# Performance work log

Measured on AMD Instinct MI355X. Metric: run time of the kernel, lower is better.

## Reference

```python
import jax, jax.numpy as jnp
import numpy as np

DIM = 256
HEADS = 8
HD = DIM // HEADS
SR = 2
SCALE = HD ** -0.5
EPS = 1e-5


def _layernorm(t, g, b):
    m = jnp.mean(t, axis=-1, keepdims=True)
    v = jnp.mean((t - m) ** 2, axis=-1, keepdims=True)
    return (t - m) / jnp.sqrt(v + EPS) * g + b


def _sr_kv(t, H, W, sr_w, sr_b, ln_g, ln_b, Wkv):
    # t: [B, N, C] with N == H*W -> spatial-reduction conv -> LN -> kv proj
    B, N, C = t.shape
    img = t.transpose(0, 2, 1).reshape(B, C, H, W)
    red = jax.lax.conv_general_dilated(
        img, sr_w, window_strides=(SR, SR), padding='VALID',
        dimension_numbers=('NCHW', 'OIHW', 'NCHW')) + sr_b[None, :, None, None]
    red = red.reshape(B, C, -1).transpose(0, 2, 1)  # [B, Nr, C]
    red = _layernorm(red, ln_g, ln_b)
    Nr = red.shape[1]
    kv = (red @ Wkv).reshape(B, Nr, 2, HEADS, HD).transpose(2, 0, 3, 1, 4)
    return kv[0], kv[1]  # k, v: [B, h, Nr, d]


def _q_heads(t, Wq):
    B, N, _ = t.shape
    return (t @ Wq).reshape(B, N, HEADS, HD).transpose(0, 2, 1, 3)  # [B,h,N,d]


def _attn_out(q, k, v, proj_w, proj_b):
    a = jnp.einsum('bhqd,bhkd->bhqk', q, k) * SCALE
    a = jax.nn.softmax(a, axis=-1)
    o = jnp.einsum('bhqk,bhkd->bhqd', a, v)
    B, h, N, d = o.shape
    return o.transpose(0, 2, 1, 3).reshape(B, N, h * d) @ proj_w + proj_b


def _forward(x, y, Wq, Wkv, sr_w, sr_b, ln_g, ln_b, proj_w, proj_b,
             H_x, W_x, H_y, W_y):
    # B_x == 1 branch of the original module (static shapes)
    B_y = y.shape[0]
    q_x = _q_heads(x, Wq)
    q_y = _q_heads(y, Wq)
    k_x, v_x = _sr_kv(x, H_x, W_x, sr_w, sr_b, ln_g, ln_b, Wkv)
    k_y, v_y = _sr_kv(y, H_y, W_y, sr_w, sr_b, ln_g, ln_b, Wkv)
    # x attends to its own KV + batch-averaged support KV
    k_cat_x = jnp.concatenate([k_x, jnp.mean(k_y, axis=0, keepdims=True)], axis=2)
    v_cat_x = jnp.concatenate([v_x, jnp.mean(v_y, axis=0, keepdims=True)], axis=2)
    x_out = _attn_out(q_x, k_cat_x, v_cat_x, proj_w, proj_b)
    # each support attends to repeated query KV + its own KV
    k_cat_y = jnp.concatenate([jnp.broadcast_to(k_x, (B_y,) + k_x.shape[1:]), k_y], axis=2)
    v_cat_y = jnp.concatenate([jnp.broadcast_to(v_x, (B_y,) + v_x.shape[1:]), v_y], axis=2)
    y_out = _attn_out(q_y, k_cat_y, v_cat_y, proj_w, proj_b)
    return x_out, y_out


def setup_inputs() -> dict:
    key = jax.random.key(0)
    ks = jax.random.split(key, 6)
    std = 0.02
    return {
        'x': jax.random.normal(ks[0], (1, 6400, DIM), jnp.float32),
        'y': jax.random.normal(ks[1], (4, 1024, DIM), jnp.float32),
        'Wq': jax.random.normal(ks[2], (DIM, DIM), jnp.float32) * std,
        'Wkv': jax.random.normal(ks[3], (DIM, 2 * DIM), jnp.float32) * std,
        'sr_w': jax.random.normal(ks[4], (DIM, DIM, SR, SR), jnp.float32) * np.sqrt(2.0 / (SR * SR * DIM)),
        'sr_b': jnp.zeros((DIM,), jnp.float32),
        'ln_g': jnp.ones((DIM,), jnp.float32),
        'ln_b': jnp.zeros((DIM,), jnp.float32),
        'proj_w': jax.random.normal(ks[5], (DIM, DIM), jnp.float32) * std,
        'proj_b': jnp.zeros((DIM,), jnp.float32),
        'H_x': 80, 'W_x': 80, 'H_y': 32, 'W_y': 32,
    }


def reference(x, y, Wq, Wkv, sr_w, sr_b, ln_g, ln_b, proj_w, proj_b,
              H_x, W_x, H_y, W_y):
    return _forward(x, y, Wq, Wkv, sr_w, sr_b, ln_g, ln_b, proj_w, proj_b,
                    H_x, W_x, H_y, W_y)
```

## Files before the change

kernel.cpp:

```cpp
#include <hip/hip_runtime.h>
#include <math.h>

#define DIM 256
#define HD 32
#define KSCALE (0.17677669529663687f * 1.44269504088896340736f)
#define EPS 1e-5f

typedef __attribute__((ext_vector_type(8))) short short8;
typedef __attribute__((ext_vector_type(4))) float f32x4;

union U8 { uint4 u; short8 s; };

__device__ inline unsigned short f2bf(float f) {
    union { float f; unsigned u; } v; v.f = f;
    unsigned r = v.u + 0x7FFF + ((v.u >> 16) & 1);
    return (unsigned short)(r >> 16);
}
__device__ inline float bf2f(unsigned short h) {
    union { unsigned u; float f; } v; v.u = ((unsigned)h) << 16;
    return v.f;
}
__device__ inline unsigned pk2bf(float a, float b) {
    unsigned ua = __float_as_uint(a) + 0x8000u;
    unsigned ub = __float_as_uint(b) + 0x8000u;
    return __builtin_amdgcn_perm(ub, ua, 0x07060302u);
}
__device__ inline uint4 pk8bf(float4 a, float4 b) {
    return make_uint4(pk2bf(a.x, a.y), pk2bf(a.z, a.w),
                      pk2bf(b.x, b.y), pk2bf(b.z, b.w));
}
__device__ inline void up2(unsigned u, float& a, float& b) {
    a = __uint_as_float(u << 16);
    b = __uint_as_float(u & 0xffff0000u);
}
__device__ inline void gl_lds16(const unsigned short* g, unsigned short* l) {
    __builtin_amdgcn_global_load_lds(
        (const __attribute__((address_space(1))) unsigned int*)g,
        (__attribute__((address_space(3))) unsigned int*)l, 16, 0, 0);
}
#define MFMA16(a, b, c) __builtin_amdgcn_mfma_f32_16x16x32_bf16(a, b, c, 0, 0, 0)
#define EXP2(x) __builtin_amdgcn_exp2f(x)

__global__ __launch_bounds__(256) void prep_w(
    const float* __restrict__ Wq, const float* __restrict__ Wkv,
    const float* __restrict__ projw, const float* __restrict__ srw,
    unsigned short* __restrict__ WqT, unsigned short* __restrict__ WkvT,
    unsigned short* __restrict__ projT, unsigned short* __restrict__ BwT,
    unsigned short* __restrict__ pads)
{
    int idx = blockIdx.x * 256 + threadIdx.x;
    if (idx < 65536) { int n = idx >> 8, k = idx & 255; WqT[idx] = f2bf(Wq[(k << 8) + n]); return; }
    idx -= 65536;
    if (idx < 131072) { int n = idx >> 8, k = idx & 255; WkvT[idx] = f2bf(Wkv[(k << 9) + n]); return; }
    idx -= 131072;
    if (idx < 65536) { int n = idx >> 8, k = idx & 255; projT[idx] = f2bf(projw[(k << 8) + n]); return; }
    idx -= 65536;
    if (idx < 262144) { int o = idx >> 10, rem = idx & 1023, q = rem >> 8, i = rem & 255;
                        BwT[idx] = f2bf(srw[(o << 10) + (i << 2) + q]); return; }
    idx -= 262144;
    pads[idx] = 0;
}

__global__ __launch_bounds__(256) void convq_kernel(
    const float* __restrict__ x, const float* __restrict__ y,
    const unsigned short* __restrict__ BwT, const unsigned short* __restrict__ WqT,
    unsigned short* __restrict__ redA, unsigned short* __restrict__ redB,
    unsigned short* __restrict__ qxb, unsigned short* __restrict__ qyb)
{
    __shared__ __align__(16) unsigned short At[128][32];
    __shared__ __align__(16) unsigned short Btile[64][32];
    const int tid = threadIdx.x;
    const int lane = tid & 63, w = tid >> 6;
    const int c = lane & 15, quad = lane >> 4;
    const int bid = blockIdx.x;

    if (bid < 328) {
        const int n0 = (bid & 3) << 6, r = bid >> 2;
        const float* Xb; int W, W2, m0g, pl, kh;
        if (r < 50) {
            const int myi = r >> 1; kh = r & 1;
            Xb = x; W = 80; W2 = 40; m0g = myi * 64; pl = myi * 64;
        } else {
            const int ry = r - 50, idx = ry >> 1; kh = ry & 1;
            const int b = idx >> 2, mt = idx & 3;
            Xb = y + (size_t)b * 262144; W = 32; W2 = 16;
            m0g = 1600 + b * 256 + mt * 64; pl = mt * 64;
        }
        unsigned short* Cb = (kh == 0) ? redA : redB;
        const int srow = tid >> 2, sch = (tid & 3) << 3;
        const int p = pl + srow;
        const int oy = p / W2, ox = p - oy * W2;
        const unsigned short* Bp = BwT + (size_t)(n0 + srow) * 1024 + sch;
        const int kbeg = kh << 9, kend = kbeg + 512;

        auto addrA = [&](int k0) {
            const int qq = k0 >> 8;
            const int rrow = (2 * oy + (qq >> 1)) * W + 2 * ox + (qq & 1);
            return Xb + (size_t)rrow * DIM + (k0 & 255) + sch;
        };

        const float* ap = addrA(kbeg);
        float4 a0 = *(const float4*)ap, a1 = *(const float4*)(ap + 4);
        uint4 bn = *(const uint4*)(Bp + kbeg);
        f32x4 acc[4] = {};
        for (int k0 = kbeg; k0 < kend; k0 += 32) {
            *(uint4*)&At[srow][sch]    = pk8bf(a0, a1);
            *(uint4*)&Btile[srow][sch] = bn;
            if (k0 < kend - 32) {
                const float* np = addrA(k0 + 32);
                a0 = *(const float4*)np; a1 = *(const float4*)(np + 4);
                bn = *(const uint4*)(Bp + k0 + 32);
            }
            __syncthreads();
            short8 a = *(short8*)&At[(w << 4) + c][quad << 3];
            #pragma unroll
            for (int nb = 0; nb < 4; ++nb) {
                short8 b = *(short8*)&Btile[(nb << 4) + c][quad << 3];
                acc[nb] = MFMA16(a, b, acc[nb]);
            }
            __syncthreads();
        }
        const int rl = (w << 4) + (quad << 2);
        #pragma unroll
        for (int nb = 0; nb < 4; ++nb) {
            const int col = n0 + (nb << 4) + c;
            #pragma unroll
            for (int rr = 0; rr < 4; ++rr)
                Cb[(size_t)(m0g + rl + rr) * DIM + col] = f2bf(acc[nb][rr]);
        }
    } else {
        const int r = bid - 328;
        const int n0 = (r & 3) << 6, mg = (r >> 2) << 7;
        const float* Ab = (mg < 6400) ? x + (size_t)mg * 256
                                      : y + (size_t)(mg - 6400) * 256;
        unsigned short* Cb = (mg < 6400) ? qxb + (size_t)mg * 256
                                         : qyb + (size_t)(mg - 6400) * 256;
        const int arow = tid >> 1, ach = (tid & 1) << 4;
        const float* Ap = Ab + (size_t)arow * 256 + ach;
        const int brow = tid >> 2, bch = (tid & 3) << 3;
        const unsigned short* Bp = WqT + (size_t)(n0 + brow) * 256 + bch;

        float4 a0 = *(const float4*)Ap,       a1 = *(const float4*)(Ap + 4);
        float4 a2 = *(const float4*)(Ap + 8), a3 = *(const float4*)(Ap + 12);
        uint4 bn = *(const uint4*)Bp;
        f32x4 acc[2][4] = {};
        for (int k0 = 0; k0 < 256; k0 += 32) {
            *(uint4*)&At[arow][ach]     = pk8bf(a0, a1);
            *(uint4*)&At[arow][ach + 8] = pk8bf(a2, a3);
            *(uint4*)&Btile[brow][bch]  = bn;
            if (k0 < 224) {
                a0 = *(const float4*)(Ap + k0 + 32); a1 = *(const float4*)(Ap + k0 + 36);
                a2 = *(const float4*)(Ap + k0 + 40); a3 = *(const float4*)(Ap + k0 + 44);
                bn = *(const uint4*)(Bp + k0 + 32);
            }
            __syncthreads();
            #pragma unroll
            for (int ml = 0; ml < 2; ++ml) {
                short8 a = *(short8*)&At[(w << 5) + (ml << 4) + c][quad << 3];
                #pragma unroll
                for (int nb = 0; nb < 4; ++nb) {
                    short8 b = *(short8*)&Btile[(nb << 4) + c][quad << 3];
                    acc[ml][nb] = MFMA16(a, b, acc[ml][nb]);
                }
            }
            __syncthreads();
        }
        #pragma unroll
        for (int ml = 0; ml < 2; ++ml) {
            const int rl = (w << 5) + (ml << 4) + (quad << 2);
            #pragma unroll
            for (int nb = 0; nb < 4; ++nb) {
                const int col = n0 + (nb << 4) + c;
                #pragma unroll
                for (int rr = 0; rr < 4; ++rr)
                    Cb[(size_t)(rl + rr) * 256 + col] = f2bf(acc[ml][nb][rr]);
            }
        }
    }
}

__global__ __launch_bounds__(256) void kvln_kernel(
    const unsigned short* __restrict__ redA, const unsigned short* __restrict__ redB,
    const unsigned short* __restrict__ WkvT, const float* __restrict__ srb,
    const float* __restrict__ g, const float* __restrict__ bta,
    unsigned short* __restrict__ kswx, unsigned short* __restrict__ vswx,
    unsigned short* __restrict__ kswy, unsigned short* __restrict__ vswy)
{
    __shared__ __align__(16) unsigned short At[64][32];
    __shared__ __align__(16) unsigned short Btile[64][32];
    const int tid = threadIdx.x;
    const int lane = tid & 63, w = tid >> 6;
    const int c = lane & 15, quad = lane >> 4;
    const int srow = tid >> 2, sch = (tid & 3) << 3;
    const int bid = blockIdx.x;
    const int n0 = (bid & 7) << 6, mg = (bid >> 3) << 6;
    const unsigned short* ArowA = redA + (size_t)(mg + srow) * 256 + sch;
    const unsigned short* ArowB = redB + (size_t)(mg + srow) * 256 + sch;

    uint4 araw[8];
    float s1 = 0.f, s2 = 0.f;
    #pragma unroll
    for (int ci = 0; ci < 8; ++ci) {
        uint4 ua = *(const uint4*)(ArowA + (ci << 5));
        uint4 ub = *(const uint4*)(ArowB + (ci << 5));
        const int ch = (ci << 5) + sch;
        float4 sb0 = *(const float4*)(srb + ch), sb1 = *(const float4*)(srb + ch + 4);
        const unsigned* dua = (const unsigned*)&ua;
        const unsigned* dub = (const unsigned*)&ub;
        float t[8];
        #pragma unroll
        for (int dd = 0; dd < 4; ++dd) {
            float a0, a1, b0, b1;
            up2(dua[dd], a0, a1); up2(dub[dd], b0, b1);
            t[2 * dd]     = a0 + b0;
            t[2 * dd + 1] = a1 + b1;
        }
        t[0] += sb0.x; t[1] += sb0.y; t[2] += sb0.z; t[3] += sb0.w;
        t[4] += sb1.x; t[5] += sb1.y; t[6] += sb1.z; t[7] += sb1.w;
        #pragma unroll
        for (int j = 0; j < 8; ++j) { s1 += t[j]; s2 += t[j] * t[j]; }
        araw[ci] = pk8bf(make_float4(t[0], t[1], t[2], t[3]),
                         make_float4(t[4], t[5], t[6], t[7]));
    }
    s1 += __shfl_xor(s1, 1); s1 += __shfl_xor(s1, 2);
    s2 += __shfl_xor(s2, 1); s2 += __shfl_xor(s2, 2);
    const float mean = s1 * (1.0f / 256.0f);
    const float var  = s2 * (1.0f / 256.0f) - mean * mean;
    const float rstd = rsqrtf(var + EPS);

    #pragma unroll
    for (int ci = 0; ci < 8; ++ci) {
        const int ch = (ci << 5) + sch;
        float4 g0 = *(const float4*)(g + ch),   g1 = *(const float4*)(g + ch + 4);
        float4 b0 = *(const float4*)(bta + ch), b1 = *(const float4*)(bta + ch + 4);
        const unsigned* du = (const unsigned*)&araw[ci];
        float v[8];
        #pragma unroll
        for (int dd = 0; dd < 4; ++dd) up2(du[dd], v[2 * dd], v[2 * dd + 1]);
        float4 o0 = make_float4(fmaf((v[0] - mean) * rstd, g0.x, b0.x),
                                fmaf((v[1] - mean) * rstd, g0.y, b0.y),
                                fmaf((v[2] - mean) * rstd, g0.z, b0.z),
                                fmaf((v[3] - mean) * rstd, g0.w, b0.w));
        float4 o1 = make_float4(fmaf((v[4] - mean) * rstd, g1.x, b1.x),
                                fmaf((v[5] - mean) * rstd, g1.y, b1.y),
                                fmaf((v[6] - mean) * rstd, g1.z, b1.z),
                                fmaf((v[7] - mean) * rstd, g1.w, b1.w));
        araw[ci] = pk8bf(o0, o1);
    }

    const unsigned short* Bp = WkvT + (size_t)(n0 + srow) * 256 + sch;
    uint4 bn = *(const uint4*)Bp;
    f32x4 acc[4] = {};
    for (int k0 = 0; k0 < 256; k0 += 32) {
        *(uint4*)&At[srow][sch]    = araw[k0 >> 5];
        *(uint4*)&Btile[srow][sch] = bn;
        if (k0 < 224) bn = *(const uint4*)(Bp + k0 + 32);
        __syncthreads();
        short8 a = *(short8*)&At[(w << 4) + c][quad << 3];
        #pragma unroll
        for (int nb = 0; nb < 4; ++nb) {
            short8 b = *(short8*)&Btile[(nb << 4) + c][quad << 3];
            acc[nb] = MFMA16(a, b, acc[nb]);
        }
        __syncthreads();
    }

    const int rl = (w << 4) + (quad << 2);
    const int r0 = mg - 1600;
    const int half = rl >> 5, kl0 = rl & 31;
    const int vkeyoff = (half << 10) + (((kl0 >> 2) & 3) << 7) + ((kl0 >> 4) << 2);
    #pragma unroll
    for (int nb = 0; nb < 4; ++nb) {
        const int col = n0 + (nb << 4) + c;
        if (col < 256) {
            const int hh = col >> 5, d = col & 31;
            unsigned short* base = (mg < 1600)
                ? kswx + ((size_t)(hh * 25 + (mg >> 6)) << 11)
                : kswy + ((size_t)(r0 >> 8) << 16) + ((size_t)((hh << 2) + ((r0 >> 6) & 3)) << 11);
            unsigned short* dst = base + (((d >> 3) << 9)) + (d & 7);
            #pragma unroll
            for (int r = 0; r < 4; ++r)
                dst[(rl + r) << 3] = f2bf(acc[nb][r] * KSCALE);
        } else {
            const int hd = col - 256, hv = hd >> 5, d = hd & 31;
            unsigned short* base = (mg < 1600)
                ? vswx + ((size_t)(hv * 25 + (mg >> 6)) << 11)
                : vswy + ((size_t)(r0 >> 8) << 16) + ((size_t)((hv << 2) + ((r0 >> 6) & 3)) << 11);
            unsigned lo = (unsigned)f2bf(acc[nb][0]) | ((unsigned)f2bf(acc[nb][1]) << 16);
            unsigned hi = (unsigned)f2bf(acc[nb][2]) | ((unsigned)f2bf(acc[nb][3]) << 16);
            *(uint2*)(base + vkeyoff + ((d >> 4) << 9) + ((d & 15) << 3)) =
                make_uint2(lo, hi);
        }
    }
}

__global__ __launch_bounds__(256) void kvmean_kernel(
    const unsigned short* __restrict__ kswy, const unsigned short* __restrict__ vswy,
    unsigned short* __restrict__ kmsw, unsigned short* __restrict__ vmsw)
{
    int idx = blockIdx.x * 256 + threadIdx.x;
    const unsigned short* s; unsigned short* dv; int e;
    if (idx < 65536) { s = kswy; dv = kmsw; e = idx; }
    else             { s = vswy; dv = vmsw; e = idx - 65536; }
    float sm = bf2f(s[e]) + bf2f(s[e + 65536]) + bf2f(s[e + 131072]) + bf2f(s[e + 196608]);
    dv[e] = f2bf(0.25f * sm);
}

__global__ __launch_bounds__(256) void attn_mfma(
    unsigned short* __restrict__ qxb, unsigned short* __restrict__ qyb,
    const unsigned short* __restrict__ kswx, const unsigned short* __restrict__ vswx,
    const unsigned short* __restrict__ kmsw, const unsigned short* __restrict__ vmsw,
    const unsigned short* __restrict__ kswy, const unsigned short* __restrict__ vswy,
    const unsigned short* __restrict__ kpad, const unsigned short* __restrict__ vpad)
{
    __shared__ __align__(16) unsigned short KV[2][8192];
    __shared__ __align__(16) float lsumLDS[4][64];

    const int tid = threadIdx.x;
    const int lane = tid & 63, w = tid >> 6;
    const int c = lane & 15, quad = lane >> 4;

    const int bid = blockIdx.x;
    unsigned short* qb; const unsigned short *k1, *v1, *k2, *v2;
    int h, qoff;
    if (bid < 800) {
        h = bid / 100; qoff = (bid - h * 100) * 64;
        qb = qxb;
        k1 = kswx + ((size_t)h * 25 << 11); v1 = vswx + ((size_t)h * 25 << 11);
        k2 = kmsw + ((size_t)h << 13);      v2 = vmsw + ((size_t)h << 13);
    } else {
        const int idx = bid - 800, b = idx >> 7, rem = idx & 127;
        h = rem >> 4; qoff = b * 1024 + (rem & 15) * 64;
        qb = qyb;
        k1 = kswx + ((size_t)h * 25 << 11); v1 = vswx + ((size_t)h * 25 << 11);
        k2 = kswy + ((size_t)b << 16) + ((size_t)h << 13);
        v2 = vswy + ((size_t)b << 16) + ((size_t)h << 13);
    }

    short8 qf[4];
    #pragma unroll
    for (int nb = 0; nb < 4; ++nb)
        qf[nb] = *(const short8*)(qb + (size_t)(qoff + (nb << 4) + c) * DIM
                                  + h * HD + (quad << 3));

    auto ksrc = [&](int t) -> const unsigned short* {
        if (t < 25) return k1 + (t << 11);
        if (t < 29) return k2 + ((t - 25) << 11);
        return kpad;
    };
    auto vsrc = [&](int t) -> const unsigned short* {
        if (t < 25) return v1 + (t << 11);
        if (t < 29) return v2 + ((t - 25) << 11);
        return vpad;
    };

    const int sg = (w << 9) + (lane << 3);
    auto stage = [&](int i, int pb) {
        #pragma unroll
        for (int tt = 0; tt < 2; ++tt) {
            const int t = 2 * i + tt;
            gl_lds16(ksrc(t) + sg, &KV[pb][(tt << 11) + (w << 9)]);
            gl_lds16(vsrc(t) + sg, &KV[pb][4096 + (tt << 11) + (w << 9)]);
        }
    };

    const int tb = w >> 1, half = w & 1;
    float lsr[4] = {0.f, 0.f, 0.f, 0.f};
    f32x4 oacc[4][2] = {};
    const f32x4 zero = {0.f, 0.f, 0.f, 0.f};

    stage(0, 0);
    __syncthreads();

    for (int i = 0; i < 15; ++i) {
        const int pb = i & 1;
        if (i < 14) stage(i + 1, pb ^ 1);

        const unsigned short* Kp = &KV[pb][(tb << 11) + (quad << 9) + (((half << 5) + c) << 3)];
        short8 ka0 = *(const short8*)(Kp);
        short8 ka1 = *(const short8*)(Kp + 128);
        f32x4 s0[4], s1[4];
        #pragma unroll
        for (int nb = 0; nb < 4; ++nb) s0[nb] = MFMA16(ka0, qf[nb], zero);
        #pragma unroll
        for (int nb = 0; nb < 4; ++nb) s1[nb] = MFMA16(ka1, qf[nb], zero);

        U8 af[4];
        #pragma unroll
        for (int nb = 0; nb < 4; ++nb) {
            float p0 = EXP2(s0[nb][0]), p1 = EXP2(s0[nb][1]);
            float p2 = EXP2(s0[nb][2]), p3 = EXP2(s0[nb][3]);
            float q0 = EXP2(s1[nb][0]), q1 = EXP2(s1[nb][1]);
            float q2 = EXP2(s1[nb][2]), q3 = EXP2(s1[nb][3]);
            lsr[nb] += ((p0 + p1) + (p2 + p3)) + ((q0 + q1) + (q2 + q3));
            af[nb].u = make_uint4(pk2bf(p0, p1), pk2bf(p2, p3),
                                  pk2bf(q0, q1), pk2bf(q2, q3));
        }

        const unsigned short* Vp = &KV[pb][4096 + (tb << 11) + (half << 10) + (quad << 7) + (c << 3)];
        short8 vb0 = *(const short8*)(Vp);
        short8 vb1 = *(const short8*)(Vp + 512);
        #pragma unroll
        for (int nb = 0; nb < 4; ++nb) {
            oacc[nb][0] = MFMA16(af[nb].s, vb0, oacc[nb][0]);
            oacc[nb][1] = MFMA16(af[nb].s, vb1, oacc[nb][1]);
        }

        __syncthreads();
    }

    #pragma unroll
    for (int nb = 0; nb < 4; ++nb) {
        lsr[nb] += __shfl_xor(lsr[nb], 16);
        lsr[nb] += __shfl_xor(lsr[nb], 32);
    }
    if (lane < 16) {
        #pragma unroll
        for (int nb = 0; nb < 4; ++nb) lsumLDS[w][(nb << 4) + lane] = lsr[nb];
    }
    float* Op = (float*)&KV[0][0];
    #pragma unroll
    for (int nb = 0; nb < 4; ++nb)
        #pragma unroll
        for (int db = 0; db < 2; ++db)
            *(f32x4*)&Op[((((w << 2) + nb) << 1) + db) * 256 + (c << 4) + (quad << 2)] =
                oacc[nb][db];
    __syncthreads();

    f32x4 lt = {0.f, 0.f, 0.f, 0.f};
    #pragma unroll
    for (int w2 = 0; w2 < 4; ++w2)
        lt += *(f32x4*)&lsumLDS[w2][(w << 4) + (quad << 2)];
    float inv[4];
    #pragma unroll
    for (int r = 0; r < 4; ++r) inv[r] = 1.0f / (lt[r] - 64.0f);
    #pragma unroll
    for (int db = 0; db < 2; ++db) {
        f32x4 o = zero;
        #pragma unroll
        for (int w2 = 0; w2 < 4; ++w2)
            o += *(f32x4*)&Op[((((w2 << 2) + w) << 1) + db) * 256 + (c << 4) + (quad << 2)];
        #pragma unroll
        for (int r = 0; r < 4; ++r) {
            const int row = qoff + (w << 4) + (quad << 2) + r;
            qb[(size_t)row * DIM + h * HD + (db << 4) + c] = f2bf(o[r] * inv[r]);
        }
    }
}

__global__ __launch_bounds__(256) void proj_mfma(
    const unsigned short* __restrict__ qxb, const unsigned short* __restrict__ qyb,
    const unsigned short* __restrict__ projT, const float* __restrict__ bias,
    float* __restrict__ outx, float* __restrict__ outy)
{
    __shared__ __align__(16) unsigned short At[128][32];
    __shared__ __align__(16) unsigned short Btile[64][32];
    const int tid = threadIdx.x;
    const int lane = tid & 63, w = tid >> 6;
    const int c = lane & 15, quad = lane >> 4;

    const int bid = blockIdx.x;
    const int n0 = (bid & 3) << 6, mg = (bid >> 2) << 7;
    const unsigned short* Ab = (mg < 6400) ? qxb + (size_t)mg * 256
                                           : qyb + (size_t)(mg - 6400) * 256;
    float* Cf = (mg < 6400) ? outx + (size_t)mg * 256 : outy + (size_t)(mg - 6400) * 256;

    const int arow = tid >> 1, ach = (tid & 1) << 4;
    const unsigned short* Ap = Ab + (size_t)arow * 256 + ach;
    const int brow = tid >> 2, bch = (tid & 3) << 3;
    const unsigned short* Bp = projT + (size_t)(n0 + brow) * 256 + bch;

    uint4 an0 = *(const uint4*)Ap, an1 = *(const uint4*)(Ap + 8);
    uint4 bn  = *(const uint4*)Bp;
    f32x4 acc[2][4] = {};
    for (int k0 = 0; k0 < 256; k0 += 32) {
        *(uint4*)&At[arow][ach]     = an0;
        *(uint4*)&At[arow][ach + 8] = an1;
        *(uint4*)&Btile[brow][bch]  = bn;
        if (k0 < 224) {
            an0 = *(const uint4*)(Ap + k0 + 32);
            an1 = *(const uint4*)(Ap + k0 + 40);
            bn  = *(const uint4*)(Bp + k0 + 32);
        }
        __syncthreads();
        #pragma unroll
        for (int ml = 0; ml < 2; ++ml) {
            short8 a = *(short8*)&At[(w << 5) + (ml << 4) + c][quad << 3];
            #pragma unroll
            for (int nb = 0; nb < 4; ++nb) {
                short8 b = *(short8*)&Btile[(nb << 4) + c][quad << 3];
                acc[ml][nb] = MFMA16(a, b, acc[ml][nb]);
            }
        }
        __syncthreads();
    }
    #pragma unroll
    for (int ml = 0; ml < 2; ++ml) {
        const int rl = (w << 5) + (ml << 4) + (quad << 2);
        #pragma unroll
        for (int nb = 0; nb < 4; ++nb) {
            const int col = n0 + (nb << 4) + c;
            const float bv = bias[col];
            #pragma unroll
            for (int r = 0; r < 4; ++r)
                Cf[(size_t)(rl + r) * 256 + col] = acc[ml][nb][r] + bv;
        }
    }
}

extern "C" void kernel_launch(void* const* d_in, const int* in_sizes, int n_in,
                              void* d_out, int out_size, void* d_ws, size_t ws_size,
                              hipStream_t stream)
{
    const float* x      = (const float*)d_in[0];
    const float* y      = (const float*)d_in[1];
    const float* Wq     = (const float*)d_in[2];
    const float* Wkv    = (const float*)d_in[3];
    const float* sr_w   = (const float*)d_in[4];
    const float* sr_b   = (const float*)d_in[5];
    const float* ln_g   = (const float*)d_in[6];
    const float* ln_b   = (const float*)d_in[7];
    const float* proj_w = (const float*)d_in[8];
    const float* proj_b = (const float*)d_in[9];

    unsigned short* p = (unsigned short*)d_ws;
    unsigned short* WqT   = p;  p += 65536;
    unsigned short* WkvT  = p;  p += 131072;
    unsigned short* projT = p;  p += 65536;
    unsigned short* BwT   = p;  p += 262144;
    unsigned short* redA  = p;  p += 671744;
    unsigned short* redB  = p;  p += 671744;
    unsigned short* qxb   = p;  p += 1638400;
    unsigned short* qyb   = p;  p += 1048576;
    unsigned short* kswx  = p;  p += 409600;
    unsigned short* vswx  = p;  p += 409600;
    unsigned short* kswy  = p;  p += 262144;
    unsigned short* vswy  = p;  p += 262144;
    unsigned short* kmsw  = p;  p += 65536;
    unsigned short* vmsw  = p;  p += 65536;
    unsigned short* kpad  = p;  p += 2048;
    unsigned short* vpad  = p;  p += 2048;
    float* outx = (float*)d_out;
    float* outy = outx + 6400 * 256;

    prep_w<<<2064, 256, 0, stream>>>(Wq, Wkv, proj_w, sr_w, WqT, WkvT, projT, BwT, kpad);
    convq_kernel<<<656, 256, 0, stream>>>(x, y, BwT, WqT, redA, redB, qxb, qyb);
    kvln_kernel<<<328, 256, 0, stream>>>(redA, redB, WkvT, sr_b, ln_g, ln_b,
                                         kswx, vswx, kswy, vswy);
    kvmean_kernel<<<512, 256, 0, stream>>>(kswy, vswy, kmsw, vmsw);
    attn_mfma<<<1312, 256, 0, stream>>>(qxb, qyb, kswx, vswx, kmsw, vmsw,
                                        kswy, vswy, kpad, vpad);
    proj_mfma<<<328, 256, 0, stream>>>(qxb, qyb, projT, proj_b, outx, outy);
}
```

Before: 166.6 us.

## Double attention query tile to 128 rows and stage KV epilogue stores through LDS

The attention kernel now processes 128 query rows per block instead of 64, halving the grid. Each K/V tile staged in LDS is therefore reused across twice as many queries, and score-exp-PV is interleaved per query block. The cross-wave output reduction runs in two passes. Separately, the kvln epilogue writes its swizzled K/V tiles into shared memory and then copies them out with 16-byte coalesced stores instead of scattered 2-byte writes. The trade-off is more registers per attention thread and fewer blocks for occupancy.

```diff
diff --git a/kernel.cpp b/kernel.cpp
--- a/kernel.cpp
+++ b/kernel.cpp
@@ -186,8 +186,7 @@
     unsigned short* __restrict__ kswx, unsigned short* __restrict__ vswx,
     unsigned short* __restrict__ kswy, unsigned short* __restrict__ vswy)
 {
-    __shared__ __align__(16) unsigned short At[64][32];
-    __shared__ __align__(16) unsigned short Btile[64][32];
+    __shared__ __align__(16) unsigned short SM[4096];
     const int tid = threadIdx.x;
     const int lane = tid & 63, w = tid >> 6;
     const int c = lane & 15, quad = lane >> 4;
@@ -252,14 +251,14 @@
     uint4 bn = *(const uint4*)Bp;
     f32x4 acc[4] = {};
     for (int k0 = 0; k0 < 256; k0 += 32) {
-        *(uint4*)&At[srow][sch]    = araw[k0 >> 5];
-        *(uint4*)&Btile[srow][sch] = bn;
+        *(uint4*)&SM[srow * 32 + sch]        = araw[k0 >> 5];
+        *(uint4*)&SM[2048 + srow * 32 + sch] = bn;
         if (k0 < 224) bn = *(const uint4*)(Bp + k0 + 32);
         __syncthreads();
-        short8 a = *(short8*)&At[(w << 4) + c][quad << 3];
+        short8 a = *(short8*)&SM[((w << 4) + c) * 32 + (quad << 3)];
         #pragma unroll
         for (int nb = 0; nb < 4; ++nb) {
-            short8 b = *(short8*)&Btile[(nb << 4) + c][quad << 3];
+            short8 b = *(short8*)&SM[2048 + ((nb << 4) + c) * 32 + (quad << 3)];
             acc[nb] = MFMA16(a, b, acc[nb]);
         }
         __syncthreads();
@@ -267,31 +266,49 @@
 
     const int rl = (w << 4) + (quad << 2);
     const int r0 = mg - 1600;
-    const int half = rl >> 5, kl0 = rl & 31;
-    const int vkeyoff = (half << 10) + (((kl0 >> 2) & 3) << 7) + ((kl0 >> 4) << 2);
-    #pragma unroll
-    for (int nb = 0; nb < 4; ++nb) {
-        const int col = n0 + (nb << 4) + c;
-        if (col < 256) {
-            const int hh = col >> 5, d = col & 31;
-            unsigned short* base = (mg < 1600)
-                ? kswx + ((size_t)(hh * 25 + (mg >> 6)) << 11)
-                : kswy + ((size_t)(r0 >> 8) << 16) + ((size_t)((hh << 2) + ((r0 >> 6) & 3)) << 11);
-            unsigned short* dst = base + (((d >> 3) << 9)) + (d & 7);
+    if (n0 < 256) {
+        #pragma unroll
+        for (int nb = 0; nb < 4; ++nb) {
+            const int col = n0 + (nb << 4) + c;
+            const int hsel = (col >> 5) & 1, d = col & 31;
+            unsigned short* q = &SM[(hsel << 11) + ((d >> 3) << 9) + (d & 7)];
             #pragma unroll
             for (int r = 0; r < 4; ++r)
-                dst[(rl + r) << 3] = f2bf(acc[nb][r] * KSCALE);
-        } else {
-            const int hd = col - 256, hv = hd >> 5, d = hd & 31;
-            unsigned short* base = (mg < 1600)
-                ? vswx + ((size_t)(hv * 25 + (mg >> 6)) << 11)
-                : vswy + ((size_t)(r0 >> 8) << 16) + ((size_t)((hv << 2) + ((r0 >> 6) & 3)) << 11);
+                q[(rl + r) << 3] = f2bf(acc[nb][r] * KSCALE);
+        }
+    } else {
+        const int half = rl >> 5, kl0 = rl & 31;
+        const int vkey = (half << 10) + (((kl0 >> 2) & 3) << 7) + ((kl0 >> 4) << 2);
+        #pragma unroll
+        for (int nb = 0; nb < 4; ++nb) {
+            const int hd = n0 - 256 + (nb << 4) + c;
+            const int vsel = (hd >> 5) & 1, d = hd & 31;
             unsigned lo = (unsigned)f2bf(acc[nb][0]) | ((unsigned)f2bf(acc[nb][1]) << 16);
             unsigned hi = (unsigned)f2bf(acc[nb][2]) | ((unsigned)f2bf(acc[nb][3]) << 16);
-            *(uint2*)(base + vkeyoff + ((d >> 4) << 9) + ((d & 15) << 3)) =
+            *(uint2*)&SM[(vsel << 11) + vkey + ((d >> 4) << 9) + ((d & 15) << 3)] =
                 make_uint2(lo, hi);
         }
     }
+    __syncthreads();
+
+    const int tsel = tid >> 7, toff = (tid & 127) << 4;
+    const unsigned short* srcp = &SM[(tsel << 11) + toff];
+    unsigned short* dstp;
+    if (n0 < 256) {
+        const int hh = (n0 >> 5) + tsel;
+        dstp = (mg < 1600)
+            ? kswx + ((size_t)(hh * 25 + (mg >> 6)) << 11) + toff
+            : kswy + ((size_t)(r0 >> 8) << 16)
+                   + ((size_t)((hh << 2) + ((r0 >> 6) & 3)) << 11) + toff;
+    } else {
+        const int hv = ((n0 - 256) >> 5) + tsel;
+        dstp = (mg < 1600)
+            ? vswx + ((size_t)(hv * 25 + (mg >> 6)) << 11) + toff
+            : vswy + ((size_t)(r0 >> 8) << 16)
+                   + ((size_t)((hv << 2) + ((r0 >> 6) & 3)) << 11) + toff;
+    }
+    *(uint4*)dstp       = *(const uint4*)srcp;
+    *(uint4*)(dstp + 8) = *(const uint4*)(srcp + 8);
 }
 
 __global__ __launch_bounds__(256) void kvmean_kernel(
@@ -314,7 +331,7 @@
     const unsigned short* __restrict__ kpad, const unsigned short* __restrict__ vpad)
 {
     __shared__ __align__(16) unsigned short KV[2][8192];
-    __shared__ __align__(16) float lsumLDS[4][64];
+    __shared__ __align__(16) float lsumLDS[4][128];
 
     const int tid = threadIdx.x;
     const int lane = tid & 63, w = tid >> 6;
@@ -323,23 +340,23 @@
     const int bid = blockIdx.x;
     unsigned short* qb; const unsigned short *k1, *v1, *k2, *v2;
     int h, qoff;
-    if (bid < 800) {
-        h = bid / 100; qoff = (bid - h * 100) * 64;
+    if (bid < 400) {
+        h = bid / 50; qoff = (bid - h * 50) * 128;
         qb = qxb;
         k1 = kswx + ((size_t)h * 25 << 11); v1 = vswx + ((size_t)h * 25 << 11);
         k2 = kmsw + ((size_t)h << 13);      v2 = vmsw + ((size_t)h << 13);
     } else {
-        const int idx = bid - 800, b = idx >> 7, rem = idx & 127;
-        h = rem >> 4; qoff = b * 1024 + (rem & 15) * 64;
+        const int idx = bid - 400, b = idx >> 6, rem = idx & 63;
+        h = rem >> 3; qoff = b * 1024 + (rem & 7) * 128;
         qb = qyb;
         k1 = kswx + ((size_t)h * 25 << 11); v1 = vswx + ((size_t)h * 25 << 11);
         k2 = kswy + ((size_t)b << 16) + ((size_t)h << 13);
         v2 = vswy + ((size_t)b << 16) + ((size_t)h << 13);
     }
 
-    short8 qf[4];
+    short8 qf[8];
     #pragma unroll
-    for (int nb = 0; nb < 4; ++nb)
+    for (int nb = 0; nb < 8; ++nb)
         qf[nb] = *(const short8*)(qb + (size_t)(qoff + (nb << 4) + c) * DIM
                                   + h * HD + (quad << 3));
 
@@ -365,8 +382,8 @@
     };
 
     const int tb = w >> 1, half = w & 1;
-    float lsr[4] = {0.f, 0.f, 0.f, 0.f};
-    f32x4 oacc[4][2] = {};
+    float lsr[8] = {};
+    f32x4 oacc[8][2] = {};
     const f32x4 zero = {0.f, 0.f, 0.f, 0.f};
 
     stage(0, 0);
@@ -379,72 +396,71 @@
         const unsigned short* Kp = &KV[pb][(tb << 11) + (quad << 9) + (((half << 5) + c) << 3)];
         short8 ka0 = *(const short8*)(Kp);
         short8 ka1 = *(const short8*)(Kp + 128);
-        f32x4 s0[4], s1[4];
-        #pragma unroll
-        for (int nb = 0; nb < 4; ++nb) s0[nb] = MFMA16(ka0, qf[nb], zero);
-        #pragma unroll
-        for (int nb = 0; nb < 4; ++nb) s1[nb] = MFMA16(ka1, qf[nb], zero);
-
-        U8 af[4];
-        #pragma unroll
-        for (int nb = 0; nb < 4; ++nb) {
-            float p0 = EXP2(s0[nb][0]), p1 = EXP2(s0[nb][1]);
-            float p2 = EXP2(s0[nb][2]), p3 = EXP2(s0[nb][3]);
-            float q0 = EXP2(s1[nb][0]), q1 = EXP2(s1[nb][1]);
-            float q2 = EXP2(s1[nb][2]), q3 = EXP2(s1[nb][3]);
-            lsr[nb] += ((p0 + p1) + (p2 + p3)) + ((q0 + q1) + (q2 + q3));
-            af[nb].u = make_uint4(pk2bf(p0, p1), pk2bf(p2, p3),
-                                  pk2bf(q0, q1), pk2bf(q2, q3));
-        }
-
         const unsigned short* Vp = &KV[pb][4096 + (tb << 11) + (half << 10) + (quad << 7) + (c << 3)];
         short8 vb0 = *(const short8*)(Vp);
         short8 vb1 = *(const short8*)(Vp + 512);
-        #pragma unroll
-        for (int nb = 0; nb < 4; ++nb) {
-            oacc[nb][0] = MFMA16(af[nb].s, vb0, oacc[nb][0]);
-            oacc[nb][1] = MFMA16(af[nb].s, vb1, oacc[nb][1]);
+
+        #pragma unroll
+        for (int nb = 0; nb < 8; ++nb) {
+            f32x4 s0 = MFMA16(ka0, qf[nb], zero);
+            f32x4 s1 = MFMA16(ka1, qf[nb], zero);
+            float p0 = EXP2(s0[0]), p1 = EXP2(s0[1]);
+            float p2 = EXP2(s0[2]), p3 = EXP2(s0[3]);
+            float q0 = EXP2(s1[0]), q1 = EXP2(s1[1]);
+            float q2 = EXP2(s1[2]), q3 = EXP2(s1[3]);
+            lsr[nb] += ((p0 + p1) + (p2 + p3)) + ((q0 + q1) + (q2 + q3));
+            U8 af;
+            af.u = make_uint4(pk2bf(p0, p1), pk2bf(p2, p3),
+                              pk2bf(q0, q1), pk2bf(q2, q3));
+            oacc[nb][0] = MFMA16(af.s, vb0, oacc[nb][0]);
+            oacc[nb][1] = MFMA16(af.s, vb1, oacc[nb][1]);
         }
 
         __syncthreads();
     }
 
     #pragma unroll
-    for (int nb = 0; nb < 4; ++nb) {
+    for (int nb = 0; nb < 8; ++nb) {
         lsr[nb] += __shfl_xor(lsr[nb], 16);
         lsr[nb] += __shfl_xor(lsr[nb], 32);
     }
     if (lane < 16) {
         #pragma unroll
-        for (int nb = 0; nb < 4; ++nb) lsumLDS[w][(nb << 4) + lane] = lsr[nb];
+        for (int nb = 0; nb < 8; ++nb) lsumLDS[w][(nb << 4) + lane] = lsr[nb];
     }
     float* Op = (float*)&KV[0][0];
+
     #pragma unroll
-    for (int nb = 0; nb < 4; ++nb)
-        #pragma unroll
-        for (int db = 0; db < 2; ++db)
-            *(f32x4*)&Op[((((w << 2) + nb) << 1) + db) * 256 + (c << 4) + (quad << 2)] =
-                oacc[nb][db];
-    __syncthreads();
-
-    f32x4 lt = {0.f, 0.f, 0.f, 0.f};
-    #pragma unroll
-    for (int w2 = 0; w2 < 4; ++w2)
-        lt += *(f32x4*)&lsumLDS[w2][(w << 4) + (quad << 2)];
-    float inv[4];
-    #pragma unroll
-    for (int r = 0; r < 4; ++r) inv[r] = 1.0f / (lt[r] - 64.0f);
-    #pragma unroll
-    for (int db = 0; db < 2; ++db) {
-        f32x4 o = zero;
+    for (int pass = 0; pass < 2; ++pass) {
+        #pragma unroll
+        for (int nb2 = 0; nb2 < 4; ++nb2)
+            #pragma unroll
+            for (int db = 0; db < 2; ++db)
+                *(f32x4*)&Op[(((w << 2) + nb2) * 2 + db) * 256 + (c << 4) + (quad << 2)] =
+                    oacc[(pass << 2) + nb2][db];
+        __syncthreads();
+
+        const int nb = (pass << 2) + w;
+        f32x4 lt = {0.f, 0.f, 0.f, 0.f};
         #pragma unroll
         for (int w2 = 0; w2 < 4; ++w2)
-            o += *(f32x4*)&Op[((((w2 << 2) + w) << 1) + db) * 256 + (c << 4) + (quad << 2)];
-        #pragma unroll
-        for (int r = 0; r < 4; ++r) {
-            const int row = qoff + (w << 4) + (quad << 2) + r;
-            qb[(size_t)row * DIM + h * HD + (db << 4) + c] = f2bf(o[r] * inv[r]);
-        }
+            lt += *(f32x4*)&lsumLDS[w2][(nb << 4) + (quad << 2)];
+        float inv[4];
+        #pragma unroll
+        for (int r = 0; r < 4; ++r) inv[r] = 1.0f / (lt[r] - 64.0f);
+        #pragma unroll
+        for (int db = 0; db < 2; ++db) {
+            f32x4 o = zero;
+            #pragma unroll
+            for (int w2 = 0; w2 < 4; ++w2)
+                o += *(f32x4*)&Op[(((w2 << 2) + w) * 2 + db) * 256 + (c << 4) + (quad << 2)];
+            #pragma unroll
+            for (int r = 0; r < 4; ++r) {
+                const int row = qoff + (nb << 4) + (quad << 2) + r;
+                qb[(size_t)row * DIM + h * HD + (db << 4) + c] = f2bf(o[r] * inv[r]);
+            }
+        }
+        __syncthreads();
     }
 }
 
@@ -548,7 +564,7 @@
     kvln_kernel<<<328, 256, 0, stream>>>(redA, redB, WkvT, sr_b, ln_g, ln_b,
                                          kswx, vswx, kswy, vswy);
     kvmean_kernel<<<512, 256, 0, stream>>>(kswy, vswy, kmsw, vmsw);
-    attn_mfma<<<1312, 256, 0, stream>>>(qxb, qyb, kswx, vswx, kmsw, vmsw,
-                                        kswy, vswy, kpad, vpad);
+    attn_mfma<<<656, 256, 0, stream>>>(qxb, qyb, kswx, vswx, kmsw, vmsw,
+                                       kswy, vswy, kpad, vpad);
     proj_mfma<<<328, 256, 0, stream>>>(qxb, qyb, projT, proj_b, outx, outy);
 }
```

Result: slower. 173.0 us (+3.9%).
